# Kernel optimization log

Measured on AMD Instinct MI355X. Metric: run time of the kernel, lower is better.

Reference implementation:

```python
import jax, jax.numpy as jnp
import numpy as np

B, N, D = 8, 900, 256
SA_H, CA_H = 8, 8
L, P = 4, 4
FF = 2048
SHAPES = ((128, 128), (64, 64), (32, 32), (16, 16))
STARTS = (0, 16384, 20480, 21504)
S = 21760
D_BAND = (D // 6) * 2   # 84
D_ROPE = 3 * D_BAND     # 252
NF = D_BAND // 2        # 42
EPS = 1e-5


def _ln(x, g, b):
    mu = jnp.mean(x, -1, keepdims=True)
    var = jnp.mean((x - mu) ** 2, -1, keepdims=True)
    return (x - mu) * jax.lax.rsqrt(var + EPS) * g + b


def _rotate_half(x):
    x1 = x[..., 0::2]
    x2 = x[..., 1::2]
    return jnp.stack([-x2, x1], axis=-1).reshape(x.shape)


def _rope(q, k, boxes):
    freqs = 1.0 / (10000.0 ** (jnp.arange(NF, dtype=jnp.float32) / NF))
    cx, cy = boxes[..., 0], boxes[..., 1]
    xy = cx * cy

    def cs(v, f):
        a = v[..., None] * f
        return jnp.repeat(jnp.cos(a), 2, -1), jnp.repeat(jnp.sin(a), 2, -1)

    cx_c, cx_s = cs(cx, freqs)
    cy_c, cy_s = cs(cy, freqs)
    xy_c, xy_s = cs(xy, freqs * 0.1)
    cos = jnp.concatenate([cx_c, cy_c, xy_c], -1)
    sin = jnp.concatenate([cx_s, cy_s, xy_s], -1)

    def app(t):
        a, rest = t[..., :D_ROPE], t[..., D_ROPE:]
        return jnp.concatenate([a * cos + _rotate_half(a) * sin, rest], -1)

    return app(q), app(k)


def _bilinear(img, xy):
    # img: (Hl, Wl, C); xy: (M, 2) normalized in [0,1]
    # torch grid_sample semantics: align_corners=False, zero padding
    Hl, Wl, _ = img.shape
    x = xy[:, 0] * Wl - 0.5
    y = xy[:, 1] * Hl - 0.5
    x0 = jnp.floor(x)
    y0 = jnp.floor(y)
    lx = x - x0
    ly = y - y0
    x0i = x0.astype(jnp.int32)
    y0i = y0.astype(jnp.int32)

    def tap(yi, xi):
        valid = (xi >= 0) & (xi < Wl) & (yi >= 0) & (yi < Hl)
        v = img[jnp.clip(yi, 0, Hl - 1), jnp.clip(xi, 0, Wl - 1)]
        return v * valid[:, None].astype(v.dtype)

    return (tap(y0i, x0i) * ((1 - ly) * (1 - lx))[:, None]
            + tap(y0i, x0i + 1) * ((1 - ly) * lx)[:, None]
            + tap(y0i + 1, x0i) * (ly * (1 - lx))[:, None]
            + tap(y0i + 1, x0i + 1) * (ly * lx)[:, None])


def _forward(tgt, memory, query_pos, ref_boxes, reference_points,
             wq, bq, wk, bk, wv, bv, sa_wo, sa_bo, n1_g, n1_b,
             off_w, off_b, aw_w, aw_b, val_w, val_b, co_w, co_b,
             n2_g, n2_b, ff1_w, ff1_b, ff2_w, ff2_b, n3_g, n3_b):
    dh = D // SA_H
    # --- self attention with ComplexRoPE2D applied pre-projection ---
    q = tgt + query_pos
    k = tgt + query_pos
    q, k = _rope(q, k, ref_boxes)
    qh = (q @ wq + bq).reshape(B, N, SA_H, dh).transpose(0, 2, 1, 3)
    kh = (k @ wk + bk).reshape(B, N, SA_H, dh).transpose(0, 2, 1, 3)
    vh = (tgt @ wv + bv).reshape(B, N, SA_H, dh).transpose(0, 2, 1, 3)
    att = jax.nn.softmax(jnp.einsum('bhqd,bhkd->bhqk', qh, kh) * (dh ** -0.5), axis=-1)
    sa = jnp.einsum('bhqk,bhkd->bhqd', att, vh).transpose(0, 2, 1, 3).reshape(B, N, D)
    tgt = _ln(tgt + sa @ sa_wo + sa_bo, n1_g, n1_b)

    # --- multi-scale deformable cross-attention ---
    cdh = D // CA_H
    q2 = tgt + query_pos
    value = (memory @ val_w + val_b).reshape(B, S, CA_H, cdh)
    off = (q2 @ off_w + off_b).reshape(B, N, CA_H, L, P, 2)
    aw = jax.nn.softmax((q2 @ aw_w + aw_b).reshape(B, N, CA_H, L * P), axis=-1)
    aw = aw.reshape(B, N, CA_H, L, P)
    # offset normalizer is (W, H) per level
    normalizer = jnp.array([[w_, h_] for (h_, w_) in SHAPES], dtype=jnp.float32)
    loc = reference_points[:, :, None, :, None, :] + off / normalizer[None, None, None, :, None, :]
    out = jnp.zeros((B, CA_H, N, cdh), dtype=tgt.dtype)
    for l, (Hl, Wl) in enumerate(SHAPES):
        st = STARTS[l]
        v_l = value[:, st:st + Hl * Wl].reshape(B, Hl, Wl, CA_H, cdh)
        v_l = v_l.transpose(0, 3, 1, 2, 4).reshape(B * CA_H, Hl, Wl, cdh)
        loc_l = loc[:, :, :, l].transpose(0, 2, 1, 3, 4).reshape(B * CA_H, N * P, 2)
        s_l = jax.vmap(_bilinear)(v_l, loc_l).reshape(B, CA_H, N, P, cdh)
        out = out + jnp.einsum('bhnpd,bnhp->bhnd', s_l, aw[:, :, :, l])
    ca = out.transpose(0, 2, 1, 3).reshape(B, N, D) @ co_w + co_b
    tgt = _ln(tgt + ca, n2_g, n2_b)

    # --- FFN ---
    ff = jax.nn.relu(tgt @ ff1_w + ff1_b) @ ff2_w + ff2_b
    return _ln(tgt + ff, n3_g, n3_b)


def setup_inputs() -> dict:
    key = jax.random.key(0)
    ks = jax.random.split(key, 16)

    def wmat(k, shape):
        return jax.random.normal(k, shape, jnp.float32) * 0.02

    z = lambda *s: jnp.zeros(s, jnp.float32)
    o = lambda *s: jnp.ones(s, jnp.float32)
    return dict(
        tgt=jax.random.normal(ks[0], (B, N, D), jnp.float32),
        memory=jax.random.normal(ks[1], (B, S, D), jnp.float32),
        query_pos=jax.random.normal(ks[2], (B, N, D), jnp.float32) * 0.02,
        ref_boxes=jax.random.uniform(ks[3], (B, N, 4), jnp.float32),
        reference_points=jax.random.uniform(ks[4], (B, N, L, 2), jnp.float32),
        wq=wmat(ks[5], (D, D)), bq=z(D),
        wk=wmat(ks[6], (D, D)), bk=z(D),
        wv=wmat(ks[7], (D, D)), bv=z(D),
        sa_wo=wmat(ks[8], (D, D)), sa_bo=z(D),
        n1_g=o(D), n1_b=z(D),
        off_w=wmat(ks[9], (D, CA_H * L * P * 2)), off_b=z(CA_H * L * P * 2),
        aw_w=wmat(ks[10], (D, CA_H * L * P)), aw_b=z(CA_H * L * P),
        val_w=wmat(ks[11], (D, D)), val_b=z(D),
        co_w=wmat(ks[12], (D, D)), co_b=z(D),
        n2_g=o(D), n2_b=z(D),
        ff1_w=wmat(ks[13], (D, FF)), ff1_b=z(FF),
        ff2_w=wmat(ks[14], (FF, D)), ff2_b=z(D),
        n3_g=o(D), n3_b=z(D))


def reference(tgt, memory, query_pos, ref_boxes, reference_points,
              wq, bq, wk, bk, wv, bv, sa_wo, sa_bo, n1_g, n1_b,
              off_w, off_b, aw_w, aw_b, val_w, val_b, co_w, co_b,
              n2_g, n2_b, ff1_w, ff1_b, ff2_w, ff2_b, n3_g, n3_b):
    return _forward(tgt, memory, query_pos, ref_boxes, reference_points,
                    wq, bq, wk, bk, wv, bv, sa_wo, sa_bo, n1_g, n1_b,
                    off_w, off_b, aw_w, aw_b, val_w, val_b, co_w, co_b,
                    n2_g, n2_b, ff1_w, ff1_b, ff2_w, ff2_b, n3_g, n3_b)
```

## Files before the change

kernel.cpp:

```cpp
#include <hip/hip_runtime.h>
#include <hip/hip_bf16.h>
#include <math.h>

#define B_ 8
#define N_ 900
#define D_ 256
#define S_ 21760
#define H_ 8
#define DH 32
#define FF_ 2048
#define NROWS (B_*N_)

typedef __attribute__((ext_vector_type(8))) short bf16x8;
typedef __attribute__((ext_vector_type(4))) float f32x4;

union BU { bf16x8 v; short s[8]; unsigned long long u[2]; };

static __device__ inline short f2bf_s(float x) {
  __hip_bfloat16 h = __float2bfloat16(x);
  return *reinterpret_cast<short*>(&h);
}

__device__ __forceinline__ void gload_lds16(const float* g, float* lds) {
  __builtin_amdgcn_global_load_lds(
      (const __attribute__((address_space(1))) void*)g,
      (__attribute__((address_space(3))) void*)lds, 16, 0, 0);
}

__global__ __launch_bounds__(128) void rope_kernel(
    const float* __restrict__ tgt, const float* __restrict__ qpos,
    const float* __restrict__ boxes, __hip_bfloat16* __restrict__ out)
{
  int row = blockIdx.x;
  int tid = threadIdx.x;
  const float* x = tgt  + (size_t)row * D_;
  const float* p = qpos + (size_t)row * D_;
  float a0 = x[2*tid]   + p[2*tid];
  float a1 = x[2*tid+1] + p[2*tid+1];
  float o0 = a0, o1 = a1;
  if (tid < 126) {
    int band = tid / 42;
    int fi   = tid - band * 42;
    float freq = powf(10000.0f, -(float)fi / 42.0f);
    float cx = boxes[(size_t)row*4 + 0];
    float cy = boxes[(size_t)row*4 + 1];
    float v  = (band == 0) ? cx : (band == 1 ? cy : cx * cy);
    if (band == 2) freq *= 0.1f;
    float ang = v * freq;
    float c = cosf(ang), s = sinf(ang);
    o0 = a0 * c - a1 * s;
    o1 = a1 * c + a0 * s;
  }
  short2 sv = make_short2(f2bf_s(o0), f2bf_s(o1));
  *(short2*)&out[(size_t)row*D_ + 2*tid] = sv;
}

__global__ __launch_bounds__(256) void wtrans_kernel(
    const float* __restrict__ wq, const float* __restrict__ wk,
    const float* __restrict__ wv, const float* __restrict__ sa_wo,
    const float* __restrict__ offw, const float* __restrict__ valw,
    const float* __restrict__ cow, const float* __restrict__ aww,
    const float* __restrict__ ff1w, const float* __restrict__ ff2w,
    short* __restrict__ Wt)
{
  int bid = blockIdx.x;
  const float* W; short* out; int K, N, tile;
  if (bid < 448) {
    int wi = bid >> 6; tile = bid & 63; K = 256; N = 256;
    const float* tab[7] = {wq, wk, wv, sa_wo, offw, valw, cow};
    const int   off[7]  = {0, 65536, 131072, 196608, 262144, 360448, 425984};
    W = tab[wi]; out = Wt + off[wi];
  } else if (bid < 480) {
    tile = bid - 448; K = 256; N = 128; W = aww; out = Wt + 327680;
  } else if (bid < 992) {
    tile = bid - 480; K = 256; N = 2048; W = ff1w; out = Wt + 491520;
  } else {
    tile = bid - 992; K = 2048; N = 256; W = ff2w; out = Wt + 1015808;
  }
  int ntn = N >> 5;
  int tk = tile / ntn, tn = tile - tk * ntn;
  __shared__ float t[32][33];
  int c = threadIdx.x & 31, rr = threadIdx.x >> 5;
  #pragma unroll
  for (int i = 0; i < 4; ++i)
    t[rr + i*8][c] = W[(size_t)(tk*32 + rr + i*8) * N + tn*32 + c];
  __syncthreads();
  #pragma unroll
  for (int i = 0; i < 4; ++i)
    out[(size_t)(tn*32 + rr + i*8) * K + tk*32 + c] = f2bf_s(t[c][rr + i*8]);
}

template<int BM, int KK, bool ABF16, bool A2ADD, bool RELU, int OUTMODE>
__global__ __launch_bounds__(256) void mgemm_kernel(
    const void* __restrict__ Ap, const float* __restrict__ A2p,
    const short* __restrict__ Wt,
    const float* __restrict__ bias, const float* __restrict__ bias2,
    void* __restrict__ Cp, void* __restrict__ Cp2, int M, int N)
{
  constexpr int MS = BM / 16;
  constexpr bool SWAP = (OUTMODE != 2);
  __shared__ short As[BM * 256];
  int tid = threadIdx.x;
  int w = tid >> 6, lane = tid & 63;
  int g = lane >> 4, r = lane & 15;
  int m0 = blockIdx.x * BM;
  int nw = blockIdx.y * 256 + w * 64;
  bool active = nw < N;

  f32x4 acc[MS][4];
  #pragma unroll
  for (int i = 0; i < MS; ++i)
    #pragma unroll
    for (int j = 0; j < 4; ++j) acc[i][j] = (f32x4){0.f,0.f,0.f,0.f};

  for (int kb = 0; kb < KK; kb += 256) {
    if (KK > 256 && kb) __syncthreads();
    #pragma unroll
    for (int i = 0; i < BM/8; ++i) {
      int u = i*256 + tid;
      int row = u >> 5, c8 = u & 31;
      BU pk;
      if (ABF16) {
        pk.v = *(const bf16x8*)((const short*)Ap + (size_t)(m0+row)*KK + kb + c8*8);
      } else {
        const float* ap = (const float*)Ap + (size_t)(m0+row)*KK + kb + c8*8;
        float4 a0 = *(const float4*)ap;
        float4 a1 = *(const float4*)(ap + 4);
        if (A2ADD) {
          const float* a2 = A2p + (size_t)(m0+row)*KK + kb + c8*8;
          float4 b0 = *(const float4*)a2;
          float4 b1 = *(const float4*)(a2 + 4);
          a0.x += b0.x; a0.y += b0.y; a0.z += b0.z; a0.w += b0.w;
          a1.x += b1.x; a1.y += b1.y; a1.z += b1.z; a1.w += b1.w;
        }
        pk.s[0]=f2bf_s(a0.x); pk.s[1]=f2bf_s(a0.y); pk.s[2]=f2bf_s(a0.z); pk.s[3]=f2bf_s(a0.w);
        pk.s[4]=f2bf_s(a1.x); pk.s[5]=f2bf_s(a1.y); pk.s[6]=f2bf_s(a1.z); pk.s[7]=f2bf_s(a1.w);
      }
      int col = (c8*8) ^ ((row & 7) << 3);
      *(bf16x8*)&As[row*256 + col] = pk.v;
    }
    __syncthreads();
    if (active) {
      #pragma unroll
      for (int kk = 0; kk < 8; ++kk) {
        BU bfr[4];
        #pragma unroll
        for (int ns = 0; ns < 4; ++ns) {
          const short* wp = Wt + (size_t)(nw + ns*16 + r)*KK + kb + kk*32;
          bfr[ns].u[0] = *(const unsigned long long*)(wp + 4*g);
          bfr[ns].u[1] = *(const unsigned long long*)(wp + 16 + 4*g);
        }
        #pragma unroll
        for (int ms = 0; ms < MS; ++ms) {
          int row = ms*16 + r;
          int c0 = (kk*32 + g*4)      ^ ((r & 7) << 3);
          int c1 = (kk*32 + 16 + g*4) ^ ((r & 7) << 3);
          BU af;
          af.u[0] = *(const unsigned long long*)&As[row*256 + c0];
          af.u[1] = *(const unsigned long long*)&As[row*256 + c1];
          #pragma unroll
          for (int ns = 0; ns < 4; ++ns) {
            if (SWAP)
              acc[ms][ns] = __builtin_amdgcn_mfma_f32_16x16x32_bf16(
                  bfr[ns].v, af.v, acc[ms][ns], 0, 0, 0);
            else
              acc[ms][ns] = __builtin_amdgcn_mfma_f32_16x16x32_bf16(
                  af.v, bfr[ns].v, acc[ms][ns], 0, 0, 0);
          }
        }
      }
    }
  }
  if (!active) return;

  #pragma unroll
  for (int ms = 0; ms < MS; ++ms) {
    #pragma unroll
    for (int ns = 0; ns < 4; ++ns) {
      if (SWAP) {
        int n0 = nw + ns*16 + g*4;
        int m  = m0 + ms*16 + r;
        float4 b4;
        if (OUTMODE == 3 || OUTMODE == 4)
          b4 = (n0 < 256) ? *(const float4*)&bias[n0]
                          : *(const float4*)&bias2[n0 - 256];
        else
          b4 = *(const float4*)&bias[n0];
        float v0 = acc[ms][ns][0] + b4.x;
        float v1 = acc[ms][ns][1] + b4.y;
        float v2 = acc[ms][ns][2] + b4.z;
        float v3 = acc[ms][ns][3] + b4.w;
        if (RELU) {
          v0 = fmaxf(v0, 0.f); v1 = fmaxf(v1, 0.f);
          v2 = fmaxf(v2, 0.f); v3 = fmaxf(v3, 0.f);
        }
        if (OUTMODE == 0) {
          *(float4*)&((float*)Cp)[(size_t)m*N + n0] = make_float4(v0,v1,v2,v3);
        } else if (OUTMODE == 1) {
          short4 sv = make_short4(f2bf_s(v0), f2bf_s(v1), f2bf_s(v2), f2bf_s(v3));
          *(short4*)&((short*)Cp)[(size_t)m*N + n0] = sv;
        } else if (OUTMODE == 3) {
          short4 sv = make_short4(f2bf_s(v0), f2bf_s(v1), f2bf_s(v2), f2bf_s(v3));
          if (n0 < 256) *(short4*)&((short*)Cp )[(size_t)m*256 + n0]       = sv;
          else          *(short4*)&((short*)Cp2)[(size_t)m*256 + (n0-256)] = sv;
        } else {
          float4 fv = make_float4(v0,v1,v2,v3);
          if (n0 < 256) *(float4*)&((float*)Cp )[(size_t)m*256 + n0]       = fv;
          else          *(float4*)&((float*)Cp2)[(size_t)m*128 + (n0-256)] = fv;
        }
      } else {
        int n = nw + ns*16 + r;
        float bsc = bias[n];
        int hh = n >> 5, dd = n & 31;
        int mb = m0 + ms*16 + g*4;
        short4 sv = make_short4(
            f2bf_s(acc[ms][ns][0] + bsc), f2bf_s(acc[ms][ns][1] + bsc),
            f2bf_s(acc[ms][ns][2] + bsc), f2bf_s(acc[ms][ns][3] + bsc));
        int bb = mb / N_, bbe = (mb + 3) / N_;
        if (bb == bbe) {
          int nn = mb - bb * N_;
          *(short4*)&((short*)Cp)[((size_t)((bb*H_ + hh)*DH + dd))*N_ + nn] = sv;
        } else {
          const short* sp = (const short*)&sv;
          #pragma unroll
          for (int j = 0; j < 4; ++j) {
            int m = mb + j;
            int b2 = m / N_, nn = m - b2 * N_;
            ((short*)Cp)[((size_t)((b2*H_ + hh)*DH + dd))*N_ + nn] = sp[j];
          }
        }
      }
    }
  }
}

__global__ __launch_bounds__(256) void vgemm_kernel(
    const float* __restrict__ Ap, const short* __restrict__ Wt,
    const float* __restrict__ bias, short* __restrict__ Cp)
{
  __shared__ float buf[8][1024];
  __shared__ float dump[1024];
  int tid = threadIdx.x;
  int w = tid >> 6, l = tid & 63;
  int g = l >> 4, r = l & 15;
  int nw = w * 64;

  BU wreg[4][8];
  #pragma unroll
  for (int ns = 0; ns < 4; ++ns) {
    const short* wp = Wt + (size_t)(nw + ns*16 + r) * 256;
    #pragma unroll
    for (int kk = 0; kk < 8; ++kk) {
      wreg[ns][kk].u[0] = *(const unsigned long long*)(wp + kk*32 + 4*g);
      wreg[ns][kk].u[1] = *(const unsigned long long*)(wp + kk*32 + 16 + 4*g);
    }
  }
  float4 bs4[4];
  #pragma unroll
  for (int ns = 0; ns < 4; ++ns) bs4[ns] = *(const float4*)&bias[nw + ns*16 + g*4];

  int srow = w*8 + (l >> 3);
  int schunk = (l & 7) ^ (srow & 7);
  const float* gbase = Ap + ((size_t)blockIdx.x*160 + srow) * 256 + schunk*4;

  #pragma unroll
  for (int t = 0; t < 6; ++t)
    gload_lds16(gbase + (t>>3)*8192 + (t&7)*32, &buf[t][w*256]);

  f32x4 acc[2][4];
  #pragma unroll
  for (int i = 0; i < 2; ++i)
    #pragma unroll
    for (int j = 0; j < 4; ++j) acc[i][j] = (f32x4){0.f,0.f,0.f,0.f};

  int bb = blockIdx.x / 136;
  int pixblk = (blockIdx.x % 136) * 160;

  for (int s = 0; s < 5; ++s) {
    #pragma unroll
    for (int c = 0; c < 8; ++c) {
      int t = s*8 + c;
      int tn = t + 6;
      if (tn < 40) gload_lds16(gbase + (tn>>3)*8192 + (tn&7)*32,
                               &buf[(c+6)&7][w*256]);
      else         gload_lds16(gbase, &dump[w*256]);
      asm volatile("s_waitcnt vmcnt(6)" ::: "memory");
      __builtin_amdgcn_s_barrier();
      const float* bp = &buf[c][0];
      #pragma unroll
      for (int ms = 0; ms < 2; ++ms) {
        int row = ms*16 + r;
        const float* rp = bp + row*32;
        float4 f0 = *(const float4*)&rp[((g    ) ^ (row & 7)) * 4];
        float4 f1 = *(const float4*)&rp[((g + 4) ^ (row & 7)) * 4];
        BU af;
        af.s[0]=f2bf_s(f0.x); af.s[1]=f2bf_s(f0.y); af.s[2]=f2bf_s(f0.z); af.s[3]=f2bf_s(f0.w);
        af.s[4]=f2bf_s(f1.x); af.s[5]=f2bf_s(f1.y); af.s[6]=f2bf_s(f1.z); af.s[7]=f2bf_s(f1.w);
        #pragma unroll
        for (int ns = 0; ns < 4; ++ns)
          acc[ms][ns] = __builtin_amdgcn_mfma_f32_16x16x32_bf16(
              wreg[ns][c].v, af.v, acc[ms][ns], 0, 0, 0);
      }
    }
    int pix0 = pixblk + s*32;
    #pragma unroll
    for (int ms = 0; ms < 2; ++ms) {
      #pragma unroll
      for (int ns = 0; ns < 4; ++ns) {
        int pix = pix0 + ms*16 + r;
        int n0  = nw + ns*16 + g*4;
        int hh = n0 >> 5, dd = n0 & 31;
        short4 sv = make_short4(
            f2bf_s(acc[ms][ns][0] + bs4[ns].x),
            f2bf_s(acc[ms][ns][1] + bs4[ns].y),
            f2bf_s(acc[ms][ns][2] + bs4[ns].z),
            f2bf_s(acc[ms][ns][3] + bs4[ns].w));
        *(short4*)&Cp[((size_t)(bb*H_ + hh)*S_ + pix)*32 + dd] = sv;
        acc[ms][ns] = (f32x4){0.f,0.f,0.f,0.f};
      }
    }
  }
}

__global__ __launch_bounds__(64) void mfma_attn_kernel(
    const __hip_bfloat16* __restrict__ Q,
    const __hip_bfloat16* __restrict__ K,
    const __hip_bfloat16* __restrict__ Vt,
    float* __restrict__ O)
{
  const int NQT = 29;
  int wid = blockIdx.x;
  int qt = wid % NQT, bh = wid / NQT;
  int b = bh >> 3, h = bh & 7;
  int lane = threadIdx.x;
  int g = lane >> 4, r = lane & 15;
  int q0 = qt * 32;
  const float scale = 0.17677669529663687f;

  union U { bf16x8 v; short s[8]; unsigned long long u64[2]; };

  U qf[2];
  #pragma unroll
  for (int qq = 0; qq < 2; ++qq) {
    int qrow = min(q0 + qq*16 + r, N_ - 1);
    const __hip_bfloat16* qp = Q + ((size_t)(b*N_ + qrow))*D_ + h*DH;
    qf[qq].u64[0] = *(const unsigned long long*)(qp + 4*g);
    qf[qq].u64[1] = *(const unsigned long long*)(qp + 16 + 4*g);
  }

  f32x4 oaccA[2], oaccB[2];
  #pragma unroll
  for (int qq = 0; qq < 2; ++qq) {
    oaccA[qq] = (f32x4){0.f,0.f,0.f,0.f};
    oaccB[qq] = (f32x4){0.f,0.f,0.f,0.f};
  }
  float m0v = -1e30f, m1v = -1e30f, l0v = 0.f, l1v = 0.f;
  const f32x4 zero = {0.f,0.f,0.f,0.f};

  const __hip_bfloat16* vbase0 = Vt + (size_t)(bh*DH + r) * N_;
  const __hip_bfloat16* vbase1 = Vt + (size_t)(bh*DH + 16 + r) * N_;

  for (int kt = 0; kt < N_; kt += 32) {
    U kf0, kf1;
    {
      int kr0 = min(kt + r, N_ - 1);
      int kr1 = min(kt + 16 + r, N_ - 1);
      const __hip_bfloat16* kp0 = K + ((size_t)(b*N_ + kr0))*D_ + h*DH;
      const __hip_bfloat16* kp1 = K + ((size_t)(b*N_ + kr1))*D_ + h*DH;
      kf0.u64[0] = *(const unsigned long long*)(kp0 + 4*g);
      kf0.u64[1] = *(const unsigned long long*)(kp0 + 16 + 4*g);
      kf1.u64[0] = *(const unsigned long long*)(kp1 + 4*g);
      kf1.u64[1] = *(const unsigned long long*)(kp1 + 16 + 4*g);
    }
    U vf0, vf1;
    vf0.u64[0] = *(const unsigned long long*)(vbase0 + kt + 4*g);
    vf0.u64[1] = *(const unsigned long long*)(vbase0 + kt + 16 + 4*g);
    vf1.u64[0] = *(const unsigned long long*)(vbase1 + kt + 4*g);
    vf1.u64[1] = *(const unsigned long long*)(vbase1 + kt + 16 + 4*g);

    #pragma unroll
    for (int qq = 0; qq < 2; ++qq) {
      f32x4 s0 = __builtin_amdgcn_mfma_f32_16x16x32_bf16(kf0.v, qf[qq].v, zero, 0, 0, 0);
      f32x4 s1 = __builtin_amdgcn_mfma_f32_16x16x32_bf16(kf1.v, qf[qq].v, zero, 0, 0, 0);
      float m = qq ? m1v : m0v;
      float lv = qq ? l1v : l0v;

      float sc[8];
      #pragma unroll
      for (int j = 0; j < 4; ++j) {
        sc[j]   = (kt + 4*g + j      < N_) ? s0[j] * scale : -1e30f;
        sc[4+j] = (kt + 16 + 4*g + j < N_) ? s1[j] * scale : -1e30f;
      }
      float mx = sc[0];
      #pragma unroll
      for (int j = 1; j < 8; ++j) mx = fmaxf(mx, sc[j]);
      mx = fmaxf(mx, __shfl_xor(mx, 16));
      mx = fmaxf(mx, __shfl_xor(mx, 32));

      float mnew = fmaxf(m, mx);
      float corr = __expf(m - mnew);
      float p[8], ps = 0.f;
      #pragma unroll
      for (int j = 0; j < 8; ++j) { p[j] = __expf(sc[j] - mnew); ps += p[j]; }
      ps += __shfl_xor(ps, 16);
      ps += __shfl_xor(ps, 32);
      lv = lv * corr + ps;
      if (qq) { m1v = mnew; l1v = lv; } else { m0v = mnew; l0v = lv; }
      #pragma unroll
      for (int j = 0; j < 4; ++j) { oaccA[qq][j] *= corr; oaccB[qq][j] *= corr; }

      U pf;
      #pragma unroll
      for (int j = 0; j < 8; ++j) pf.s[j] = f2bf_s(p[j]);

      oaccA[qq] = __builtin_amdgcn_mfma_f32_16x16x32_bf16(vf0.v, pf.v, oaccA[qq], 0, 0, 0);
      oaccB[qq] = __builtin_amdgcn_mfma_f32_16x16x32_bf16(vf1.v, pf.v, oaccB[qq], 0, 0, 0);
    }
  }

  #pragma unroll
  for (int qq = 0; qq < 2; ++qq) {
    int qrow = q0 + qq*16 + r;
    if (qrow < N_) {
      float inv = 1.0f / (qq ? l1v : l0v);
      float* op = O + ((size_t)(b*N_ + qrow))*D_ + h*DH;
      #pragma unroll
      for (int j = 0; j < 4; ++j) {
        op[4*g + j]      = oaccA[qq][j] * inv;
        op[16 + 4*g + j] = oaccB[qq][j] * inv;
      }
    }
  }
}

__global__ __launch_bounds__(256) void add_ln_kernel(
    const float* __restrict__ X, const float* __restrict__ Y,
    const float* __restrict__ g, const float* __restrict__ beta,
    float* __restrict__ out)
{
  int row = blockIdx.x, tid = threadIdx.x;
  float v = X[(size_t)row*D_ + tid] + Y[(size_t)row*D_ + tid];
  float s = v, s2 = v*v;
  #pragma unroll
  for (int off = 32; off; off >>= 1) {
    s  += __shfl_down(s,  off, 64);
    s2 += __shfl_down(s2, off, 64);
  }
  __shared__ float red[8];
  int wid = tid >> 6, lane = tid & 63;
  if (lane == 0) { red[wid] = s; red[wid+4] = s2; }
  __syncthreads();
  if (tid == 0) {
    float ts  = red[0]+red[1]+red[2]+red[3];
    float ts2 = red[4]+red[5]+red[6]+red[7];
    float mu  = ts * (1.0f/D_);
    float var = ts2 * (1.0f/D_) - mu*mu;
    red[0] = mu;
    red[1] = rsqrtf(fmaxf(var, 0.0f) + 1e-5f);
  }
  __syncthreads();
  float mu = red[0], rr = red[1];
  out[(size_t)row*D_ + tid] = (v - mu)*rr*g[tid] + beta[tid];
}

__global__ __launch_bounds__(256) void sample4_kernel(
    const __hip_bfloat16* __restrict__ V, const float* __restrict__ offp,
    const float* __restrict__ awl, const float* __restrict__ refp,
    float* __restrict__ out)
{
  int tid = threadIdx.x;
  int q = tid >> 6, t = tid & 63;
  int row = blockIdx.x * 4 + q;
  int b = row / N_;
  __shared__ float s_aw[4][128];
  __shared__ float s_loc[4][256];
  #pragma unroll
  for (int i = 0; i < 2; ++i)
    s_aw[q][t + i*64] = awl[(size_t)row*128 + t + i*64];
  {
    const float norms[4] = {128.f, 64.f, 32.f, 16.f};
    #pragma unroll
    for (int i = 0; i < 4; ++i) {
      int e = t + i*64;
      int rem = e & 31, li = rem >> 3, ax = rem & 1;
      s_loc[q][e] = refp[((size_t)row*4 + li)*2 + ax]
                  + offp[(size_t)row*256 + e] / norms[li];
    }
  }
  __syncthreads();
  if (t < 8) {
    float mx = -1e30f;
    for (int j = 0; j < 16; ++j) mx = fmaxf(mx, s_aw[q][t*16+j]);
    float sum = 0.f;
    for (int j = 0; j < 16; ++j) sum += __expf(s_aw[q][t*16+j] - mx);
    float inv = 1.0f / sum;
    for (int j = 0; j < 16; ++j)
      s_aw[q][t*16+j] = __expf(s_aw[q][t*16+j] - mx) * inv;
  }
  __syncthreads();
  int h = t >> 3, dq = t & 7;
  const int dims[4]   = {128, 64, 32, 16};
  const int starts[4] = {0, 16384, 20480, 21504};
  const __hip_bfloat16* Vb = V + ((size_t)(b*H_ + h) * S_) * 32 + dq*4;
  float a0 = 0.f, a1 = 0.f, a2 = 0.f, a3 = 0.f;
  #pragma unroll
  for (int l = 0; l < 4; ++l) {
    int Wl = dims[l], st = starts[l];
    #pragma unroll
    for (int p = 0; p < 4; ++p) {
      float lx = s_loc[q][h*32 + l*8 + p*2 + 0];
      float ly = s_loc[q][h*32 + l*8 + p*2 + 1];
      float x = lx * Wl - 0.5f, y = ly * Wl - 0.5f;
      float x0f = floorf(x), y0f = floorf(y);
      float fx = x - x0f, fy = y - y0f;
      int x0 = (int)x0f, y0 = (int)y0f;
      float v0 = 0.f, v1 = 0.f, v2 = 0.f, v3 = 0.f;
      #pragma unroll
      for (int ty = 0; ty < 2; ++ty) {
        int yi = y0 + ty;
        float wy = ty ? fy : (1.f - fy);
        if (yi < 0 || yi >= Wl) continue;
        #pragma unroll
        for (int txi = 0; txi < 2; ++txi) {
          int xi = x0 + txi;
          float wx = txi ? fx : (1.f - fx);
          if (xi < 0 || xi >= Wl) continue;
          unsigned long long vv =
              *(const unsigned long long*)&Vb[(size_t)(st + yi*Wl + xi) * 32];
          float ww = wy * wx;
          v0 += ww * __uint_as_float((unsigned)(vv) << 16);
          v1 += ww * __uint_as_float((unsigned)(vv) & 0xffff0000u);
          v2 += ww * __uint_as_float((unsigned)(vv >> 32) << 16);
          v3 += ww * __uint_as_float((unsigned)(vv >> 32) & 0xffff0000u);
        }
      }
      float aw = s_aw[q][h*16 + l*4 + p];
      a0 += aw * v0; a1 += aw * v1; a2 += aw * v2; a3 += aw * v3;
    }
  }
  float4 res = make_float4(a0, a1, a2, a3);
  *(float4*)&out[(size_t)row*D_ + h*DH + dq*4] = res;
}

extern "C" void kernel_launch(void* const* d_in, const int* in_sizes, int n_in,
                              void* d_out, int out_size, void* d_ws, size_t ws_size,
                              hipStream_t stream)
{
  const float* tgt    = (const float*)d_in[0];
  const float* memory = (const float*)d_in[1];
  const float* qpos   = (const float*)d_in[2];
  const float* boxes  = (const float*)d_in[3];
  const float* refp   = (const float*)d_in[4];
  const float* wq = (const float*)d_in[5];   const float* bq = (const float*)d_in[6];
  const float* wk = (const float*)d_in[7];   const float* bk = (const float*)d_in[8];
  const float* wv = (const float*)d_in[9];   const float* bv = (const float*)d_in[10];
  const float* sa_wo = (const float*)d_in[11]; const float* sa_bo = (const float*)d_in[12];
  const float* n1g = (const float*)d_in[13]; const float* n1b = (const float*)d_in[14];
  const float* off_w = (const float*)d_in[15]; const float* off_b = (const float*)d_in[16];
  const float* aw_w  = (const float*)d_in[17]; const float* aw_b  = (const float*)d_in[18];
  const float* val_w = (const float*)d_in[19]; const float* val_b = (const float*)d_in[20];
  const float* co_w  = (const float*)d_in[21]; const float* co_b  = (const float*)d_in[22];
  const float* n2g = (const float*)d_in[23]; const float* n2b = (const float*)d_in[24];
  const float* ff1_w = (const float*)d_in[25]; const float* ff1_b = (const float*)d_in[26];
  const float* ff2_w = (const float*)d_in[27]; const float* ff2_b = (const float*)d_in[28];
  const float* n3g = (const float*)d_in[29]; const float* n3b = (const float*)d_in[30];

  char* ws = (char*)d_ws;
  size_t NE = (size_t)NROWS * D_;
  __hip_bfloat16* Vv = (__hip_bfloat16*)ws;
  __hip_bfloat16* FFM = (__hip_bfloat16*)ws;
  size_t p = (size_t)B_ * S_ * D_ * sizeof(__hip_bfloat16);
  float* A  = (float*)(ws + p); p += NE*4;
  float* Qb = (float*)(ws + p); p += NE*4;
  float* Kb = (float*)(ws + p); p += NE*4;
  float* Vh = (float*)(ws + p); p += NE*4;
  float* S1 = (float*)(ws + p); p += NE*4;
  float* S2 = (float*)(ws + p); p += NE*4;
  float* T1 = (float*)(ws + p); p += NE*4;
  short* Wt = (short*)((char*)Kb + NE*2);
  float* out = (float*)d_out;
  (void)ws_size; (void)in_sizes; (void)n_in; (void)out_size;

  const short* qk_t  = Wt;
  const short* wv_t  = Wt + 131072;
  const short* sa_t  = Wt + 196608;
  const short* offaw_t = Wt + 262144;
  const short* val_t = Wt + 360448;
  const short* co_t  = Wt + 425984;
  const short* ff1_t = Wt + 491520;
  const short* ff2_t = Wt + 1015808;

  wtrans_kernel<<<1504, 256, 0, stream>>>(wq, wk, wv, sa_wo, off_w, val_w,
                                          co_w, aw_w, ff1_w, ff2_w, Wt);

  rope_kernel<<<NROWS, 128, 0, stream>>>(tgt, qpos, boxes, (__hip_bfloat16*)A);
  mgemm_kernel<32,256,true,false,false,3><<<dim3(225,2), 256, 0, stream>>>(
      A, nullptr, qk_t, bq, bk, Qb, Kb, NROWS, 512);
  mgemm_kernel<32,256,false,false,false,2><<<dim3(225,1), 256, 0, stream>>>(
      tgt, nullptr, wv_t, bv, nullptr, Vh, nullptr, NROWS, 256);
  mfma_attn_kernel<<<29 * B_ * H_, 64, 0, stream>>>(
      (const __hip_bfloat16*)Qb, (const __hip_bfloat16*)Kb,
      (const __hip_bfloat16*)Vh, S1);
  mgemm_kernel<32,256,false,false,false,0><<<dim3(225,1), 256, 0, stream>>>(
      S1, nullptr, sa_t, sa_bo, nullptr, S2, nullptr, NROWS, 256);
  add_ln_kernel<<<NROWS, 256, 0, stream>>>(tgt, S2, n1g, n1b, T1);

  vgemm_kernel<<<1088, 256, 0, stream>>>(memory, val_t, val_b, (short*)Vv);
  mgemm_kernel<32,256,false,true,false,4><<<dim3(225,2), 256, 0, stream>>>(
      T1, qpos, offaw_t, off_b, aw_b, Qb, Kb, NROWS, 384);
  sample4_kernel<<<NROWS/4, 256, 0, stream>>>(Vv, Qb, Kb, refp, S1);
  mgemm_kernel<32,256,false,false,false,0><<<dim3(225,1), 256, 0, stream>>>(
      S1, nullptr, co_t, co_b, nullptr, S2, nullptr, NROWS, 256);
  add_ln_kernel<<<NROWS, 256, 0, stream>>>(T1, S2, n2g, n2b, T1);

  mgemm_kernel<32,256,false,false,true,1><<<dim3(225,8), 256, 0, stream>>>(
      T1, nullptr, ff1_t, ff1_b, nullptr, FFM, nullptr, NROWS, FF_);
  mgemm_kernel<32,2048,true,false,false,0><<<dim3(225,1), 256, 0, stream>>>(
      FFM, nullptr, ff2_t, ff2_b, nullptr, S2, nullptr, NROWS, 256);
  add_ln_kernel<<<NROWS, 256, 0, stream>>>(T1, S2, n3g, n3b, out);
}
```

Before: 438.4 us.

## Replace LDS-staged async pipeline in value GEMM with direct global loads

```diff
diff --git a/kernel.cpp b/kernel.cpp
--- a/kernel.cpp
+++ b/kernel.cpp
@@ -19,12 +19,6 @@
 static __device__ inline short f2bf_s(float x) {
   __hip_bfloat16 h = __float2bfloat16(x);
   return *reinterpret_cast<short*>(&h);
-}
-
-__device__ __forceinline__ void gload_lds16(const float* g, float* lds) {
-  __builtin_amdgcn_global_load_lds(
-      (const __attribute__((address_space(1))) void*)g,
-      (__attribute__((address_space(3))) void*)lds, 16, 0, 0);
 }
 
 __global__ __launch_bounds__(128) void rope_kernel(
@@ -238,8 +232,6 @@
     const float* __restrict__ Ap, const short* __restrict__ Wt,
     const float* __restrict__ bias, short* __restrict__ Cp)
 {
-  __shared__ float buf[8][1024];
-  __shared__ float dump[1024];
   int tid = threadIdx.x;
   int w = tid >> 6, l = tid & 63;
   int g = l >> 4, r = l & 15;
@@ -259,65 +251,37 @@
   #pragma unroll
   for (int ns = 0; ns < 4; ++ns) bs4[ns] = *(const float4*)&bias[nw + ns*16 + g*4];
 
-  int srow = w*8 + (l >> 3);
-  int schunk = (l & 7) ^ (srow & 7);
-  const float* gbase = Ap + ((size_t)blockIdx.x*160 + srow) * 256 + schunk*4;
-
-  #pragma unroll
-  for (int t = 0; t < 6; ++t)
-    gload_lds16(gbase + (t>>3)*8192 + (t&7)*32, &buf[t][w*256]);
-
-  f32x4 acc[2][4];
-  #pragma unroll
-  for (int i = 0; i < 2; ++i)
-    #pragma unroll
-    for (int j = 0; j < 4; ++j) acc[i][j] = (f32x4){0.f,0.f,0.f,0.f};
-
   int bb = blockIdx.x / 136;
   int pixblk = (blockIdx.x % 136) * 160;
 
-  for (int s = 0; s < 5; ++s) {
+  for (int it = 0; it < 10; ++it) {
+    int pix = pixblk + it*16 + r;
+    const float* arow = Ap + ((size_t)(blockIdx.x*160 + it*16 + r)) * 256 + 4*g;
+    f32x4 acc[4];
+    #pragma unroll
+    for (int ns = 0; ns < 4; ++ns) acc[ns] = (f32x4){0.f,0.f,0.f,0.f};
     #pragma unroll
     for (int c = 0; c < 8; ++c) {
-      int t = s*8 + c;
-      int tn = t + 6;
-      if (tn < 40) gload_lds16(gbase + (tn>>3)*8192 + (tn&7)*32,
-                               &buf[(c+6)&7][w*256]);
-      else         gload_lds16(gbase, &dump[w*256]);
-      asm volatile("s_waitcnt vmcnt(6)" ::: "memory");
-      __builtin_amdgcn_s_barrier();
-      const float* bp = &buf[c][0];
-      #pragma unroll
-      for (int ms = 0; ms < 2; ++ms) {
-        int row = ms*16 + r;
-        const float* rp = bp + row*32;
-        float4 f0 = *(const float4*)&rp[((g    ) ^ (row & 7)) * 4];
-        float4 f1 = *(const float4*)&rp[((g + 4) ^ (row & 7)) * 4];
-        BU af;
-        af.s[0]=f2bf_s(f0.x); af.s[1]=f2bf_s(f0.y); af.s[2]=f2bf_s(f0.z); af.s[3]=f2bf_s(f0.w);
-        af.s[4]=f2bf_s(f1.x); af.s[5]=f2bf_s(f1.y); af.s[6]=f2bf_s(f1.z); af.s[7]=f2bf_s(f1.w);
-        #pragma unroll
-        for (int ns = 0; ns < 4; ++ns)
-          acc[ms][ns] = __builtin_amdgcn_mfma_f32_16x16x32_bf16(
-              wreg[ns][c].v, af.v, acc[ms][ns], 0, 0, 0);
-      }
-    }
-    int pix0 = pixblk + s*32;
-    #pragma unroll
-    for (int ms = 0; ms < 2; ++ms) {
-      #pragma unroll
-      for (int ns = 0; ns < 4; ++ns) {
-        int pix = pix0 + ms*16 + r;
-        int n0  = nw + ns*16 + g*4;
-        int hh = n0 >> 5, dd = n0 & 31;
-        short4 sv = make_short4(
-            f2bf_s(acc[ms][ns][0] + bs4[ns].x),
-            f2bf_s(acc[ms][ns][1] + bs4[ns].y),
-            f2bf_s(acc[ms][ns][2] + bs4[ns].z),
-            f2bf_s(acc[ms][ns][3] + bs4[ns].w));
-        *(short4*)&Cp[((size_t)(bb*H_ + hh)*S_ + pix)*32 + dd] = sv;
-        acc[ms][ns] = (f32x4){0.f,0.f,0.f,0.f};
-      }
+      float4 f0 = *(const float4*)(arow + c*32);
+      float4 f1 = *(const float4*)(arow + c*32 + 16);
+      BU af;
+      af.s[0]=f2bf_s(f0.x); af.s[1]=f2bf_s(f0.y); af.s[2]=f2bf_s(f0.z); af.s[3]=f2bf_s(f0.w);
+      af.s[4]=f2bf_s(f1.x); af.s[5]=f2bf_s(f1.y); af.s[6]=f2bf_s(f1.z); af.s[7]=f2bf_s(f1.w);
+      #pragma unroll
+      for (int ns = 0; ns < 4; ++ns)
+        acc[ns] = __builtin_amdgcn_mfma_f32_16x16x32_bf16(
+            wreg[ns][c].v, af.v, acc[ns], 0, 0, 0);
+    }
+    #pragma unroll
+    for (int ns = 0; ns < 4; ++ns) {
+      int n0 = nw + ns*16 + g*4;
+      int hh = n0 >> 5, dd = n0 & 31;
+      short4 sv = make_short4(
+          f2bf_s(acc[ns][0] + bs4[ns].x),
+          f2bf_s(acc[ns][1] + bs4[ns].y),
+          f2bf_s(acc[ns][2] + bs4[ns].z),
+          f2bf_s(acc[ns][3] + bs4[ns].w));
+      *(short4*)&Cp[((size_t)(bb*H_ + hh)*S_ + pix)*32 + dd] = sv;
     }
   }
 }
```

New measurement: 529.2 us. 1.21x slower.
